# Kernel tuning notes

Measured on AMD Instinct MI355X. Metric: run time of the kernel, lower is better.

## Reference

```python
import jax, jax.numpy as jnp
import numpy as np
import math

N, E, K, D = 100000, 200000, 4, 8      # nodes, hyperedges, edge order, node degree (E*K == N*D)
FEAT, RANK, HID, OUT = 256, 64, 512, 128


def setup_inputs() -> dict:
    key = jax.random.key(0)
    ks = jax.random.split(key, 9)
    # D permutations of the node set, chunked into edges of K distinct nodes each
    rng = np.random.default_rng(0)
    edge_nodes = jnp.asarray(
        np.concatenate([rng.permutation(N).reshape(-1, K) for _ in range(D)], axis=0),
        dtype=jnp.int64 if jax.config.jax_enable_x64 else jnp.int32)
    sp = math.sqrt(1.0 / (FEAT + 1))
    inputs = {
        'embedding': jax.random.normal(ks[0], (N, FEAT), jnp.float32),
        'Wp': sp * jax.random.normal(ks[1], (FEAT, RANK), jnp.float32),
        'bp': jnp.zeros((RANK,), jnp.float32),
        'Wq': jax.random.normal(ks[2], (RANK, OUT), jnp.float32) / math.sqrt(RANK),
        'bq': jnp.zeros((OUT,), jnp.float32),
        'W1': jax.random.normal(ks[3], (FEAT, HID), jnp.float32) / math.sqrt(FEAT),
        'b1': jnp.zeros((HID,), jnp.float32),
        'W2': jax.random.normal(ks[4], (HID, OUT), jnp.float32) / math.sqrt(HID),
        'b2': jnp.zeros((OUT,), jnp.float32),
        'edge_nodes': edge_nodes,
    }
    return inputs


def _exclusive_prod(g):
    # g: [E, K, r] -> leave-one-out product along axis 1
    ones = jnp.ones_like(g[:, :1])
    left = jnp.concatenate([ones, jnp.cumprod(g[:, :-1], axis=1)], axis=1)
    gr = jnp.flip(g, axis=1)
    right = jnp.flip(jnp.concatenate([ones, jnp.cumprod(gr[:, :-1], axis=1)], axis=1), axis=1)
    return left * right


def reference(embedding, Wp, bp, Wq, bq, W1, b1, W2, b2, edge_nodes):
    n, _ = embedding.shape
    e, k = edge_nodes.shape
    deg = (e * k) // n                         # uniform node degree D
    num = float(deg) ** (1.0 / k)              # degree^(1/node_num), uniform
    inv_fact = 1.0 / math.factorial(k - 1)
    # p_network / p2_network (dropout = identity in eval mode)
    emb1 = embedding @ Wp + bp                 # [N, r]
    emb2 = jax.nn.relu(embedding @ W1 + b1) @ W2 + b2  # [N, out]
    scaled = num * emb1                        # deg^(1/K) * p(x_u), folded per node
    g = scaled[edge_nodes]                     # [E, K, r]
    excl = _exclusive_prod(g)                  # product over edge members != v
    term = jnp.tanh(inv_fact * num * excl)     # tanh(1/(K-1)! * deg_v^(1/K) * edge_emb)
    q_out = jnp.einsum('ekr,ro->eko', term, Wq) + bq     # q_network per (edge, member)
    edge2 = jnp.sum(emb2[edge_nodes], axis=1)            # [E, out], sum over ALL members
    contrib = q_out + jax.nn.relu(edge2)[:, None, :]     # [E, K, out]
    summed = jax.ops.segment_sum(contrib.reshape(e * k, -1),
                                 edge_nodes.reshape(-1), num_segments=n)
    return jax.nn.relu(summed / deg)           # mean over the D edges of each node, then ReLU
```

## Files before the change

kernel.cpp:

```cpp
#include <hip/hip_runtime.h>
#include <hip/hip_bf16.h>
#include <math.h>

#define NN   100000
#define EE   200000
#define KK   4
#define DEG  8
#define FEAT 256
#define RANK 64
#define HID  512
#define OUTD 128
#define EPB  25000

#define NUMF  1.6817928305074290861f
#define COEF  0.28029880508457151435f

typedef __attribute__((ext_vector_type(8))) short short8;
typedef __attribute__((ext_vector_type(4))) short short4v;
typedef __attribute__((ext_vector_type(2))) short short2v;
typedef __attribute__((ext_vector_type(4))) float float4v;

__device__ __forceinline__ short f2bf(float x) {
    union { float f; unsigned u; } v; v.f = x;
    unsigned r = v.u + 0x7fff + ((v.u >> 16) & 1);
    return (short)(r >> 16);
}
__device__ __forceinline__ float bf2f(short u) {
    union { unsigned u; float f; } v;
    v.u = ((unsigned)(unsigned short)u) << 16;
    return v.f;
}

__global__ __launch_bounds__(256) void pack_w(
    const float* __restrict__ Wp, const float* __restrict__ W1,
    const float* __restrict__ W2,
    short* __restrict__ bWp, short* __restrict__ bW1, short* __restrict__ bW2)
{
    int g = blockIdx.x * 256 + threadIdx.x;
    int tile = g >> 6, l = g & 63;
    int lm = l & 15, lq = l >> 4;
    const float* src; short* dst; int N, kt, nt, tl;
    if (tile < 32)       { tl = tile;        nt = tl >> 3; kt = tl & 7;  src = Wp; dst = bWp; N = RANK; }
    else if (tile < 288) { tl = tile - 32;   nt = tl >> 3; kt = tl & 7;  src = W1; dst = bW1; N = HID;  }
    else                 { tl = tile - 288;  nt = tl >> 4; kt = tl & 15; src = W2; dst = bW2; N = OUTD; }
    short8 pk;
    #pragma unroll
    for (int j = 0; j < 8; ++j)
        pk[j] = f2bf(src[(size_t)(kt * 32 + lq * 8 + j) * N + nt * 16 + lm]);
    *reinterpret_cast<short8*>(dst + (size_t)(tl * 64 + l) * 8) = pk;
}

__global__ __launch_bounds__(256) void node_net_mfma(
    const float* __restrict__ emb,
    const short8* __restrict__ bWp, const float* __restrict__ bp,
    const short8* __restrict__ bW1, const float* __restrict__ b1,
    const short8* __restrict__ bW2, const float* __restrict__ b2,
    short* __restrict__ scaled_b, short* __restrict__ emb2_b)
{
    __shared__ short s_a[32][264];
    __shared__ short s_h[32][136];

    const int t = threadIdx.x;
    const int w = t >> 6, l = t & 63;
    const int lm = l & 15, lq = l >> 4;
    const int row0 = blockIdx.x * 32;

    for (int i = t; i < 32 * 32; i += 256) {
        int r = i >> 5, c8 = (i & 31) * 8;
        const float4* src = reinterpret_cast<const float4*>(emb + (size_t)(row0 + r) * FEAT + c8);
        float4 v0 = src[0], v1 = src[1];
        short8 pk;
        pk[0] = f2bf(v0.x); pk[1] = f2bf(v0.y); pk[2] = f2bf(v0.z); pk[3] = f2bf(v0.w);
        pk[4] = f2bf(v1.x); pk[5] = f2bf(v1.y); pk[6] = f2bf(v1.z); pk[7] = f2bf(v1.w);
        *reinterpret_cast<short8*>(&s_a[r][c8]) = pk;
    }
    __syncthreads();

    {
        float4v acc0 = {0.f, 0.f, 0.f, 0.f}, acc1 = {0.f, 0.f, 0.f, 0.f};
        #pragma unroll
        for (int kt = 0; kt < 8; ++kt) {
            short8 e0 = *reinterpret_cast<const short8*>(&s_a[lm][kt * 32 + lq * 8]);
            short8 e1 = *reinterpret_cast<const short8*>(&s_a[16 + lm][kt * 32 + lq * 8]);
            short8 wv = bWp[(w * 8 + kt) * 64 + l];
            acc0 = __builtin_amdgcn_mfma_f32_16x16x32_bf16(wv, e0, acc0, 0, 0, 0);
            acc1 = __builtin_amdgcn_mfma_f32_16x16x32_bf16(wv, e1, acc1, 0, 0, 0);
        }
        const int cb = w * 16 + lq * 4;
        float4 bb = *reinterpret_cast<const float4*>(bp + cb);
        short4v o0 = { f2bf(NUMF * (acc0[0] + bb.x)), f2bf(NUMF * (acc0[1] + bb.y)),
                       f2bf(NUMF * (acc0[2] + bb.z)), f2bf(NUMF * (acc0[3] + bb.w)) };
        short4v o1 = { f2bf(NUMF * (acc1[0] + bb.x)), f2bf(NUMF * (acc1[1] + bb.y)),
                       f2bf(NUMF * (acc1[2] + bb.z)), f2bf(NUMF * (acc1[3] + bb.w)) };
        *reinterpret_cast<short4v*>(scaled_b + (size_t)(row0 + lm) * RANK + cb)      = o0;
        *reinterpret_cast<short4v*>(scaled_b + (size_t)(row0 + 16 + lm) * RANK + cb) = o1;
    }

    float4v eacc[2][2];
    #pragma unroll
    for (int mt = 0; mt < 2; ++mt)
        #pragma unroll
        for (int n2 = 0; n2 < 2; ++n2)
            eacc[mt][n2] = (float4v){0.f, 0.f, 0.f, 0.f};

    for (int cc = 0; cc < 4; ++cc) {
        #pragma unroll
        for (int nt2 = 0; nt2 < 2; ++nt2) {
            float4v h0 = {0.f, 0.f, 0.f, 0.f}, h1 = {0.f, 0.f, 0.f, 0.f};
            const int gnt = cc * 8 + w * 2 + nt2;
            #pragma unroll
            for (int kt = 0; kt < 8; ++kt) {
                short8 e0 = *reinterpret_cast<const short8*>(&s_a[lm][kt * 32 + lq * 8]);
                short8 e1 = *reinterpret_cast<const short8*>(&s_a[16 + lm][kt * 32 + lq * 8]);
                short8 wv = bW1[(gnt * 8 + kt) * 64 + l];
                h0 = __builtin_amdgcn_mfma_f32_16x16x32_bf16(wv, e0, h0, 0, 0, 0);
                h1 = __builtin_amdgcn_mfma_f32_16x16x32_bf16(wv, e1, h1, 0, 0, 0);
            }
            const int col  = w * 32 + nt2 * 16 + lq * 4;
            float4 bb = *reinterpret_cast<const float4*>(b1 + cc * 128 + col);
            short4v o0 = { f2bf(fmaxf(h0[0] + bb.x, 0.f)), f2bf(fmaxf(h0[1] + bb.y, 0.f)),
                           f2bf(fmaxf(h0[2] + bb.z, 0.f)), f2bf(fmaxf(h0[3] + bb.w, 0.f)) };
            short4v o1 = { f2bf(fmaxf(h1[0] + bb.x, 0.f)), f2bf(fmaxf(h1[1] + bb.y, 0.f)),
                           f2bf(fmaxf(h1[2] + bb.z, 0.f)), f2bf(fmaxf(h1[3] + bb.w, 0.f)) };
            *reinterpret_cast<short4v*>(&s_h[lm][col])      = o0;
            *reinterpret_cast<short4v*>(&s_h[16 + lm][col]) = o1;
        }
        __syncthreads();

        #pragma unroll
        for (int kt2 = 0; kt2 < 4; ++kt2) {
            short8 hh0 = *reinterpret_cast<const short8*>(&s_h[lm][kt2 * 32 + lq * 8]);
            short8 hh1 = *reinterpret_cast<const short8*>(&s_h[16 + lm][kt2 * 32 + lq * 8]);
            const int gk = cc * 4 + kt2;
            #pragma unroll
            for (int n2 = 0; n2 < 2; ++n2) {
                short8 wv = bW2[((w * 2 + n2) * 16 + gk) * 64 + l];
                eacc[0][n2] = __builtin_amdgcn_mfma_f32_16x16x32_bf16(wv, hh0, eacc[0][n2], 0, 0, 0);
                eacc[1][n2] = __builtin_amdgcn_mfma_f32_16x16x32_bf16(wv, hh1, eacc[1][n2], 0, 0, 0);
            }
        }
        __syncthreads();
    }

    #pragma unroll
    for (int n2 = 0; n2 < 2; ++n2) {
        const int col = w * 32 + n2 * 16 + lq * 4;
        float4 bb = *reinterpret_cast<const float4*>(b2 + col);
        #pragma unroll
        for (int mt = 0; mt < 2; ++mt) {
            short4v o = { f2bf(eacc[mt][n2][0] + bb.x), f2bf(eacc[mt][n2][1] + bb.y),
                          f2bf(eacc[mt][n2][2] + bb.z), f2bf(eacc[mt][n2][3] + bb.w) };
            *reinterpret_cast<short4v*>(emb2_b + (size_t)(row0 + mt * 16 + lm) * OUTD + col) = o;
        }
    }
}

__global__ __launch_bounds__(256) void edge_sum(
    const short* __restrict__ emb2_b, const int* __restrict__ edge_nodes,
    short* __restrict__ edge2r)
{
    const int t = threadIdx.x;
    const int w = t >> 6, l = t & 63;
    const int c = 2 * l;
    const int e0 = blockIdx.x * 32 + w * 8;
    #pragma unroll
    for (int it = 0; it < 8; ++it) {
        const int e = e0 + it;
        const int4 nd = *reinterpret_cast<const int4*>(edge_nodes + (size_t)e * KK);
        short2v u0 = *reinterpret_cast<const short2v*>(emb2_b + (size_t)nd.x * OUTD + c);
        short2v u1 = *reinterpret_cast<const short2v*>(emb2_b + (size_t)nd.y * OUTD + c);
        short2v u2 = *reinterpret_cast<const short2v*>(emb2_b + (size_t)nd.z * OUTD + c);
        short2v u3 = *reinterpret_cast<const short2v*>(emb2_b + (size_t)nd.w * OUTD + c);
        float s0 = bf2f(u0[0]) + bf2f(u1[0]) + bf2f(u2[0]) + bf2f(u3[0]);
        float s1 = bf2f(u0[1]) + bf2f(u1[1]) + bf2f(u2[1]) + bf2f(u3[1]);
        short2v o = { f2bf(fmaxf(s0, 0.f)), f2bf(fmaxf(s1, 0.f)) };
        *reinterpret_cast<short2v*>(edge2r + (size_t)e * OUTD + c) = o;
    }
}

__global__ __launch_bounds__(256) void make_nbr(
    const int* __restrict__ edge_nodes, int4* __restrict__ nbr)
{
    int i = blockIdx.x * 256 + threadIdx.x;
    int e = i >> 2, k = i & 3;
    const int4 nd = *reinterpret_cast<const int4*>(edge_nodes + (size_t)e * KK);
    int n  = (k == 0) ? nd.x : (k == 1) ? nd.y : (k == 2) ? nd.z : nd.w;
    int o0 = (k == 0) ? nd.y : nd.x;
    int o1 = (k <= 1) ? nd.z : nd.y;
    int o2 = (k <= 2) ? nd.w : nd.z;
    int d = e / EPB;
    nbr[(size_t)n * 8 + d] = make_int4(o0, o1, o2, e);
}

__global__ __launch_bounds__(256, 4) void node_out(
    const short* __restrict__ scaled_b, const short* __restrict__ edge2r,
    const int4* __restrict__ nbr,
    const float* __restrict__ Wq, const float* __restrict__ bq,
    float* __restrict__ out)
{
    __shared__ short s_wq[RANK * OUTD];
    __shared__ float s_t[4][64];

    const int t = threadIdx.x;
    for (int i = t; i < RANK * OUTD / 4; i += 256) {
        float4 v = reinterpret_cast<const float4*>(Wq)[i];
        short2v p0 = { f2bf(v.x), f2bf(v.y) };
        short2v p1 = { f2bf(v.z), f2bf(v.w) };
        *reinterpret_cast<short2v*>(&s_wq[i * 4])     = p0;
        *reinterpret_cast<short2v*>(&s_wq[i * 4 + 2]) = p1;
    }
    __syncthreads();

    const int w = t >> 6, l = t & 63;
    const int c = 2 * l;
    const int n = blockIdx.x * 4 + w;

    int4 nb[8];
    #pragma unroll
    for (int d = 0; d < 8; ++d) nb[d] = nbr[(size_t)n * 8 + d];

    float tsum = 0.f, s0 = 0.f, s1 = 0.f;
    #pragma unroll
    for (int d = 0; d < 8; ++d) {
        float g1 = bf2f(scaled_b[(size_t)nb[d].x * RANK + l]);
        float g2 = bf2f(scaled_b[(size_t)nb[d].y * RANK + l]);
        float g3 = bf2f(scaled_b[(size_t)nb[d].z * RANK + l]);
        short2v u = *reinterpret_cast<const short2v*>(edge2r + (size_t)nb[d].w * OUTD + c);
        tsum += tanhf(COEF * (g1 * (g2 * g3)));
        s0 += bf2f(u[0]);
        s1 += bf2f(u[1]);
    }
    s_t[w][l] = tsum;

    float q0 = 0.f, q1 = 0.f;
    #pragma unroll 8
    for (int r = 0; r < 64; ++r) {
        float tv = s_t[w][r];
        short2v wv = *reinterpret_cast<const short2v*>(&s_wq[r * OUTD + c]);
        q0 = fmaf(tv, bf2f(wv[0]), q0);
        q1 = fmaf(tv, bf2f(wv[1]), q1);
    }
    float2 bb = *reinterpret_cast<const float2*>(bq + c);
    float2 o;
    o.x = fmaxf(fmaf(0.125f, q0 + s0, bb.x), 0.f);
    o.y = fmaxf(fmaf(0.125f, q1 + s1, bb.y), 0.f);
    *reinterpret_cast<float2*>(out + (size_t)n * OUTD + c) = o;
}

extern "C" void kernel_launch(void* const* d_in, const int* in_sizes, int n_in,
                              void* d_out, int out_size, void* d_ws, size_t ws_size,
                              hipStream_t stream)
{
    const float* emb = (const float*)d_in[0];
    const float* Wp  = (const float*)d_in[1];
    const float* bp  = (const float*)d_in[2];
    const float* Wq  = (const float*)d_in[3];
    const float* bq  = (const float*)d_in[4];
    const float* W1  = (const float*)d_in[5];
    const float* b1  = (const float*)d_in[6];
    const float* W2  = (const float*)d_in[7];
    const float* b2  = (const float*)d_in[8];
    const int* edge_nodes = (const int*)d_in[9];
    float* out = (float*)d_out;

    short* scaled_b = (short*)d_ws;
    short* emb2_b   = scaled_b + (size_t)NN * RANK;
    short* edge2r   = emb2_b + (size_t)NN * OUTD;
    short* bWp      = edge2r + (size_t)EE * OUTD;
    short* bW1      = bWp + 256 * 64;
    short* bW2      = bW1 + 256 * 512;
    int4*  nbr      = (int4*)emb2_b;

    pack_w<<<104, 256, 0, stream>>>(Wp, W1, W2, bWp, bW1, bW2);
    node_net_mfma<<<NN / 32, 256, 0, stream>>>(
        emb, (const short8*)bWp, bp, (const short8*)bW1, b1, (const short8*)bW2, b2,
        scaled_b, emb2_b);
    edge_sum<<<EE / 32, 256, 0, stream>>>(emb2_b, edge_nodes, edge2r);
    make_nbr<<<EE * KK / 256, 256, 0, stream>>>(edge_nodes, nbr);
    node_out<<<NN / 4, 256, 0, stream>>>(scaled_b, edge2r, nbr, Wq, bq, out);
}
```

Baseline: 414.1 us.

## Use MFMA for Wq projection in node_out with prepacked bf16 Wq

node_out now handles 16 nodes per block instead of 4. Each wave gathers four nodes and stores the tanh sums (as bf16) and the edge sums in shared memory, then the 16x64 by 64x128 q-projection runs on bf16 MFMA using Wq that pack_w packs once up front. This removes the per-block conversion of Wq into LDS and the scalar FMA loop. tanhf is also replaced by an exp/rcp approximation, which adds some rounding error to the tanh terms and their bf16-quantised sums.

```diff
diff --git a/kernel.cpp b/kernel.cpp
--- a/kernel.cpp
+++ b/kernel.cpp
@@ -30,11 +30,16 @@
     v.u = ((unsigned)(unsigned short)u) << 16;
     return v.f;
 }
+__device__ __forceinline__ float fast_tanh(float y) {
+    float ez = __expf(2.f * y);
+    return 1.f - 2.f * __builtin_amdgcn_rcpf(ez + 1.f);
+}
 
 __global__ __launch_bounds__(256) void pack_w(
     const float* __restrict__ Wp, const float* __restrict__ W1,
-    const float* __restrict__ W2,
-    short* __restrict__ bWp, short* __restrict__ bW1, short* __restrict__ bW2)
+    const float* __restrict__ W2, const float* __restrict__ Wq,
+    short* __restrict__ bWp, short* __restrict__ bW1,
+    short* __restrict__ bW2, short* __restrict__ bWq)
 {
     int g = blockIdx.x * 256 + threadIdx.x;
     int tile = g >> 6, l = g & 63;
@@ -42,7 +47,8 @@
     const float* src; short* dst; int N, kt, nt, tl;
     if (tile < 32)       { tl = tile;        nt = tl >> 3; kt = tl & 7;  src = Wp; dst = bWp; N = RANK; }
     else if (tile < 288) { tl = tile - 32;   nt = tl >> 3; kt = tl & 7;  src = W1; dst = bW1; N = HID;  }
-    else                 { tl = tile - 288;  nt = tl >> 4; kt = tl & 15; src = W2; dst = bW2; N = OUTD; }
+    else if (tile < 416) { tl = tile - 288;  nt = tl >> 4; kt = tl & 15; src = W2; dst = bW2; N = OUTD; }
+    else                 { tl = tile - 416;  nt = tl >> 1; kt = tl & 1;  src = Wq; dst = bWq; N = OUTD; }
     short8 pk;
     #pragma unroll
     for (int j = 0; j < 8; ++j)
@@ -195,56 +201,63 @@
 __global__ __launch_bounds__(256, 4) void node_out(
     const short* __restrict__ scaled_b, const short* __restrict__ edge2r,
     const int4* __restrict__ nbr,
-    const float* __restrict__ Wq, const float* __restrict__ bq,
+    const short8* __restrict__ bWq, const float* __restrict__ bq,
     float* __restrict__ out)
 {
-    __shared__ short s_wq[RANK * OUTD];
-    __shared__ float s_t[4][64];
+    __shared__ short s_t[16][72];
+    __shared__ float s_s[16][132];
 
     const int t = threadIdx.x;
-    for (int i = t; i < RANK * OUTD / 4; i += 256) {
-        float4 v = reinterpret_cast<const float4*>(Wq)[i];
-        short2v p0 = { f2bf(v.x), f2bf(v.y) };
-        short2v p1 = { f2bf(v.z), f2bf(v.w) };
-        *reinterpret_cast<short2v*>(&s_wq[i * 4])     = p0;
-        *reinterpret_cast<short2v*>(&s_wq[i * 4 + 2]) = p1;
+    const int w = t >> 6, l = t & 63;
+    const int lm = l & 15, lq = l >> 4;
+    const int c = 2 * l;
+    const int nbase = blockIdx.x * 16;
+
+    #pragma unroll
+    for (int j = 0; j < 4; ++j) {
+        const int n = nbase + w * 4 + j;
+        int4 nb[8];
+        #pragma unroll
+        for (int d = 0; d < 8; ++d) nb[d] = nbr[(size_t)n * 8 + d];
+
+        float tsum = 0.f, s0 = 0.f, s1 = 0.f;
+        #pragma unroll
+        for (int d = 0; d < 8; ++d) {
+            float g1 = bf2f(scaled_b[(size_t)nb[d].x * RANK + l]);
+            float g2 = bf2f(scaled_b[(size_t)nb[d].y * RANK + l]);
+            float g3 = bf2f(scaled_b[(size_t)nb[d].z * RANK + l]);
+            short2v u = *reinterpret_cast<const short2v*>(edge2r + (size_t)nb[d].w * OUTD + c);
+            tsum += fast_tanh(COEF * (g1 * (g2 * g3)));
+            s0 += bf2f(u[0]);
+            s1 += bf2f(u[1]);
+        }
+        s_t[w * 4 + j][l] = f2bf(tsum);
+        *reinterpret_cast<float2*>(&s_s[w * 4 + j][c]) = make_float2(s0, s1);
     }
     __syncthreads();
 
-    const int w = t >> 6, l = t & 63;
-    const int c = 2 * l;
-    const int n = blockIdx.x * 4 + w;
-
-    int4 nb[8];
-    #pragma unroll
-    for (int d = 0; d < 8; ++d) nb[d] = nbr[(size_t)n * 8 + d];
-
-    float tsum = 0.f, s0 = 0.f, s1 = 0.f;
-    #pragma unroll
-    for (int d = 0; d < 8; ++d) {
-        float g1 = bf2f(scaled_b[(size_t)nb[d].x * RANK + l]);
-        float g2 = bf2f(scaled_b[(size_t)nb[d].y * RANK + l]);
-        float g3 = bf2f(scaled_b[(size_t)nb[d].z * RANK + l]);
-        short2v u = *reinterpret_cast<const short2v*>(edge2r + (size_t)nb[d].w * OUTD + c);
-        tsum += tanhf(COEF * (g1 * (g2 * g3)));
-        s0 += bf2f(u[0]);
-        s1 += bf2f(u[1]);
-    }
-    s_t[w][l] = tsum;
-
-    float q0 = 0.f, q1 = 0.f;
-    #pragma unroll 8
-    for (int r = 0; r < 64; ++r) {
-        float tv = s_t[w][r];
-        short2v wv = *reinterpret_cast<const short2v*>(&s_wq[r * OUTD + c]);
-        q0 = fmaf(tv, bf2f(wv[0]), q0);
-        q1 = fmaf(tv, bf2f(wv[1]), q1);
-    }
-    float2 bb = *reinterpret_cast<const float2*>(bq + c);
-    float2 o;
-    o.x = fmaxf(fmaf(0.125f, q0 + s0, bb.x), 0.f);
-    o.y = fmaxf(fmaf(0.125f, q1 + s1, bb.y), 0.f);
-    *reinterpret_cast<float2*>(out + (size_t)n * OUTD + c) = o;
+    float4v acc0 = {0.f, 0.f, 0.f, 0.f}, acc1 = {0.f, 0.f, 0.f, 0.f};
+    #pragma unroll
+    for (int kt = 0; kt < 2; ++kt) {
+        short8 tf = *reinterpret_cast<const short8*>(&s_t[lm][kt * 32 + lq * 8]);
+        short8 w0 = bWq[((w * 2 + 0) * 2 + kt) * 64 + l];
+        short8 w1 = bWq[((w * 2 + 1) * 2 + kt) * 64 + l];
+        acc0 = __builtin_amdgcn_mfma_f32_16x16x32_bf16(w0, tf, acc0, 0, 0, 0);
+        acc1 = __builtin_amdgcn_mfma_f32_16x16x32_bf16(w1, tf, acc1, 0, 0, 0);
+    }
+    #pragma unroll
+    for (int n2 = 0; n2 < 2; ++n2) {
+        float4v a = n2 ? acc1 : acc0;
+        const int col = w * 32 + n2 * 16 + lq * 4;
+        float4 sv = *reinterpret_cast<const float4*>(&s_s[lm][col]);
+        float4 bb = *reinterpret_cast<const float4*>(bq + col);
+        float4 o;
+        o.x = fmaxf(fmaf(0.125f, a[0] + sv.x, bb.x), 0.f);
+        o.y = fmaxf(fmaf(0.125f, a[1] + sv.y, bb.y), 0.f);
+        o.z = fmaxf(fmaf(0.125f, a[2] + sv.z, bb.z), 0.f);
+        o.w = fmaxf(fmaf(0.125f, a[3] + sv.w, bb.w), 0.f);
+        *reinterpret_cast<float4*>(out + (size_t)(nbase + lm) * OUTD + col) = o;
+    }
 }
 
 extern "C" void kernel_launch(void* const* d_in, const int* in_sizes, int n_in,
@@ -269,13 +282,14 @@
     short* bWp      = edge2r + (size_t)EE * OUTD;
     short* bW1      = bWp + 256 * 64;
     short* bW2      = bW1 + 256 * 512;
+    short* bWq      = bW2 + 512 * 128;
     int4*  nbr      = (int4*)emb2_b;
 
-    pack_w<<<104, 256, 0, stream>>>(Wp, W1, W2, bWp, bW1, bW2);
+    pack_w<<<108, 256, 0, stream>>>(Wp, W1, W2, Wq, bWp, bW1, bW2, bWq);
     node_net_mfma<<<NN / 32, 256, 0, stream>>>(
         emb, (const short8*)bWp, bp, (const short8*)bW1, b1, (const short8*)bW2, b2,
         scaled_b, emb2_b);
     edge_sum<<<EE / 32, 256, 0, stream>>>(emb2_b, edge_nodes, edge2r);
     make_nbr<<<EE * KK / 256, 256, 0, stream>>>(edge_nodes, nbr);
-    node_out<<<NN / 4, 256, 0, stream>>>(scaled_b, edge2r, nbr, Wq, bq, out);
-}
+    node_out<<<NN / 16, 256, 0, stream>>>(scaled_b, edge2r, nbr, (const short8*)bWq, bq, out);
+}
```

Result: faster. 354.4 us (-14.4%).
